# Optimization experiments

Measured on AMD Instinct MI355X. Metric: run time of the kernel, lower is better.

Reference implementation:

```python
import jax, jax.numpy as jnp
import numpy as np

N, CS, CZ = 512, 384, 128
H, C, PQ, PV = 12, 16, 4, 8
NB = 8
EPS = 1e-8


def _ln(x, g, b):
    m = jnp.mean(x, axis=-1, keepdims=True)
    v = jnp.mean((x - m) ** 2, axis=-1, keepdims=True)
    return (x - m) / jnp.sqrt(v + 1e-5) * g + b


def _quat_rot(bcd):
    # (1, b, c, d) quaternion -> rotation matrix, as in AF2 BackboneUpdate
    ones = jnp.ones(bcd.shape[:-1] + (1,), bcd.dtype)
    q = jnp.concatenate([ones, bcd], axis=-1)
    q = q / jnp.linalg.norm(q, axis=-1, keepdims=True)
    w, x, y, z = q[..., 0], q[..., 1], q[..., 2], q[..., 3]
    R = jnp.stack([
        1 - 2 * (y * y + z * z), 2 * (x * y - w * z), 2 * (x * z + w * y),
        2 * (x * y + w * z), 1 - 2 * (x * x + z * z), 2 * (y * z - w * x),
        2 * (x * z - w * y), 2 * (y * z + w * x), 1 - 2 * (x * x + y * y),
    ], axis=-1)
    return R.reshape(bcd.shape[:-1] + (3, 3))


def _ipa(s, z, R, t, p):
    n = s.shape[0]
    q = (s @ p['w_q']).reshape(n, H, C)
    kv = (s @ p['w_kv']).reshape(n, H, 2, C)
    k, v = kv[..., 0, :], kv[..., 1, :]

    # local points -> global frames
    q_pts = (s @ p['w_qpts']).reshape(n, H * PQ, 3)
    q_pts = jnp.einsum('nxy,npy->npx', R, q_pts) + t[:, None, :]
    q_pts = q_pts.reshape(n, H, PQ, 3)
    kv_pts = (s @ p['w_kvpts']).reshape(n, H * (PQ + PV), 3)
    kv_pts = jnp.einsum('nxy,npy->npx', R, kv_pts) + t[:, None, :]
    kv_pts = kv_pts.reshape(n, H, PQ + PV, 3)
    k_pts, v_pts = kv_pts[:, :, :PQ], kv_pts[:, :, PQ:]

    b = z @ p['w_b']  # [i, j, H]

    scalar = jnp.einsum('ihc,jhc->hij', q, k) / np.sqrt(C)
    # sum_p ||q_ip - k_jp||^2 expanded to avoid [N,N,H,P,3] intermediate
    sq_q = jnp.sum(q_pts ** 2, axis=(-1, -2)).T  # [H, i]
    sq_k = jnp.sum(k_pts ** 2, axis=(-1, -2)).T  # [H, j]
    cross = jnp.einsum('ihpc,jhpc->hij', q_pts, k_pts)
    d2 = sq_q[:, :, None] + sq_k[:, None, :] - 2.0 * cross  # [H, i, j]

    gamma = jax.nn.softplus(p['head_weights'])  # [H]
    w_C = np.sqrt(2.0 / (9.0 * PQ))
    w_L = np.sqrt(1.0 / 3.0)
    logits = w_L * (scalar + jnp.transpose(b, (2, 0, 1))
                    - gamma[:, None, None] * (w_C / 2.0) * d2)
    a = jax.nn.softmax(logits, axis=-1)  # [H, i, j]

    o = jnp.einsum('hij,jhc->ihc', a, v).reshape(n, H * C)
    o_pt = jnp.einsum('hij,jhpc->ihpc', a, v_pts)
    # back to local frame: R_i^{-1} (o_pt - t_i)
    o_pt = jnp.einsum('nyx,nhpy->nhpx', R, o_pt - t[:, None, None, :])
    o_pt_norm = jnp.sqrt(jnp.sum(o_pt ** 2, axis=-1) + EPS)  # [n, H, PV]
    o_pair = jnp.einsum('hij,ijz->ihz', a, z).reshape(n, H * CZ)

    cat = jnp.concatenate([o, o_pt.reshape(n, H * PV * 3),
                           o_pt_norm.reshape(n, H * PV), o_pair], axis=-1)
    return cat @ p['w_out'] + p['b_out']


def _forward(s, z, p):
    n = s.shape[0]
    R = jnp.broadcast_to(jnp.eye(3, dtype=s.dtype), (n, 3, 3))
    t = jnp.zeros((n, 3), s.dtype)
    for _ in range(NB):  # shared weights across blocks, as in AF2
        s = s + _ipa(s, z, R, t, p)
        s = _ln(s, p['ln1_g'], p['ln1_b'])
        h = jax.nn.relu(s @ p['w_t1'])
        h = jax.nn.relu(h @ p['w_t2'])
        s = s + h @ p['w_t3']
        s = _ln(s, p['ln2_g'], p['ln2_b'])
        upd = s @ p['w_bb'] + p['b_bb']  # [n, 6]
        Ru = _quat_rot(upd[:, :3])
        tu = upd[:, 3:]
        t = jnp.einsum('nxy,ny->nx', R, tu) + t
        R = jnp.einsum('nxy,nyz->nxz', R, Ru)
    return jnp.concatenate([s, t], axis=-1)  # [n, CS + 3]


def setup_inputs() -> dict:
    key = jax.random.key(0)
    ks = jax.random.split(key, 12)
    sc = 0.02
    cat_dim = H * C + H * PV * 3 + H * PV + H * CZ  # 2112
    return {
        's': jax.random.normal(ks[0], (N, CS), jnp.float32),
        'z': jax.random.normal(ks[1], (N, N, CZ), jnp.float32),
        'w_q': jax.random.normal(ks[2], (CS, H * C), jnp.float32) * sc,
        'w_kv': jax.random.normal(ks[3], (CS, H * 2 * C), jnp.float32) * sc,
        'w_qpts': jax.random.normal(ks[4], (CS, H * PQ * 3), jnp.float32) * sc,
        'w_kvpts': jax.random.normal(ks[5], (CS, H * (PQ + PV) * 3), jnp.float32) * sc,
        'w_b': jax.random.normal(ks[6], (CZ, H), jnp.float32) * sc,
        'head_weights': jnp.zeros((H,), jnp.float32),
        'w_out': jax.random.normal(ks[7], (cat_dim, CS), jnp.float32) * sc,
        'b_out': jnp.zeros((CS,), jnp.float32),
        'ln1_g': jnp.ones((CS,), jnp.float32),
        'ln1_b': jnp.zeros((CS,), jnp.float32),
        'w_t1': jax.random.normal(ks[8], (CS, CS), jnp.float32) * sc,
        'w_t2': jax.random.normal(ks[9], (CS, CS), jnp.float32) * sc,
        'w_t3': jax.random.normal(ks[10], (CS, CS), jnp.float32) * sc,
        'ln2_g': jnp.ones((CS,), jnp.float32),
        'ln2_b': jnp.zeros((CS,), jnp.float32),
        'w_bb': jax.random.normal(ks[11], (CS, 6), jnp.float32) * sc,
        'b_bb': jnp.zeros((6,), jnp.float32),
    }


def reference(s, z, w_q, w_kv, w_qpts, w_kvpts, w_b, head_weights, w_out,
              b_out, ln1_g, ln1_b, w_t1, w_t2, w_t3, ln2_g, ln2_b, w_bb, b_bb):
    p = dict(w_q=w_q, w_kv=w_kv, w_qpts=w_qpts, w_kvpts=w_kvpts, w_b=w_b,
             head_weights=head_weights, w_out=w_out, b_out=b_out,
             ln1_g=ln1_g, ln1_b=ln1_b, w_t1=w_t1, w_t2=w_t2, w_t3=w_t3,
             ln2_g=ln2_g, ln2_b=ln2_b, w_bb=w_bb, b_bb=b_bb)
    return _forward(s, z, p)
```

## Files before the change

kernel.cpp:

```cpp
#include <hip/hip_runtime.h>
#include <hip/hip_bf16.h>

constexpr int Nres = 512;
constexpr int Cs   = 384;
constexpr int Cz   = 128;
constexpr int NH   = 12;
constexpr int HC   = 16;
constexpr int NPQ  = 4;
constexpr int NPV  = 8;
constexpr int NBLK = 8;
constexpr int PROJD = NH*HC + NH*2*HC + NH*NPQ*3 + NH*(NPQ+NPV)*3;
constexpr int CATD = NH*HC + NH*NPV*3 + NH*NPV + NH*Cz;
constexpr float W_L  = 0.57735026918962576f;
constexpr float W_C2 = 0.11785113019775793f;

using u16 = unsigned short;
typedef __bf16 bf16x8 __attribute__((ext_vector_type(8)));
typedef float  f32x4  __attribute__((ext_vector_type(4)));

static inline int gdiv(int n, int b) { return (n + b - 1) / b; }

static __device__ __forceinline__ u16 f2bf(float x) {
    __hip_bfloat16 h = __float2bfloat16(x);
    return *reinterpret_cast<u16*>(&h);
}
static __device__ __forceinline__ float bf2f(u16 x) {
    return __bfloat162float(*reinterpret_cast<__hip_bfloat16*>(&x));
}

__global__ void k_init(const float* __restrict__ s_in, float* __restrict__ s_cur,
                       u16* __restrict__ s_bf,
                       float* __restrict__ R, float* __restrict__ t) {
    int idx = blockIdx.x * blockDim.x + threadIdx.x;
    if (idx < Nres * Cs) { float v = s_in[idx]; s_cur[idx] = v; s_bf[idx] = f2bf(v); }
    if (idx < Nres * 9) {
        int e = idx % 9;
        R[idx] = (e == 0 || e == 4 || e == 8) ? 1.f : 0.f;
    }
    if (idx < Nres * 3) t[idx] = 0.f;
}

__global__ void k_concatW(const float* __restrict__ w_q, const float* __restrict__ w_kv,
                          const float* __restrict__ w_qpts, const float* __restrict__ w_kvpts,
                          float* __restrict__ Wcat) {
    int idx = blockIdx.x * blockDim.x + threadIdx.x;
    if (idx >= Cs * PROJD) return;
    int k = idx / PROJD, n = idx - k * PROJD;
    float v;
    if      (n < 192) v = w_q[k * 192 + n];
    else if (n < 576) v = w_kv[k * 384 + (n - 192)];
    else if (n < 720) v = w_qpts[k * 144 + (n - 576)];
    else              v = w_kvpts[k * 432 + (n - 720)];
    Wcat[idx] = v;
}

__global__ void k_transposeW(const float* __restrict__ in, u16* __restrict__ out,
                             int K, int N) {
    __shared__ float tile[32][33];
    int n0 = blockIdx.x * 32, k0 = blockIdx.y * 32;
    int tx = threadIdx.x & 31, ty = threadIdx.x >> 5;
#pragma unroll
    for (int j = 0; j < 4; j++)
        tile[ty + j * 8][tx] = in[(size_t)(k0 + ty + j * 8) * N + n0 + tx];
    __syncthreads();
#pragma unroll
    for (int j = 0; j < 4; j++)
        out[(size_t)(n0 + ty + j * 8) * K + k0 + tx] = f2bf(tile[tx][ty + j * 8]);
}

__global__ void k_zT(const float* __restrict__ z, u16* __restrict__ zT) {
    __shared__ float tile[32][33];
    int i  = blockIdx.x;
    int j0 = blockIdx.y * 32;
    int c0 = blockIdx.z * 32;
    int tx = threadIdx.x & 31, ty = threadIdx.x >> 5;
    const float* src = z + (size_t)i * Nres * Cz;
#pragma unroll
    for (int l = 0; l < 4; l++)
        tile[ty + l * 8][tx] = src[(size_t)(j0 + ty + l * 8) * Cz + c0 + tx];
    __syncthreads();
    u16* dst = zT + (size_t)i * Cz * Nres;
#pragma unroll
    for (int l = 0; l < 4; l++)
        dst[(size_t)(c0 + ty + l * 8) * Nres + j0 + tx] = f2bf(tile[tx][ty + l * 8]);
}

__global__ void __launch_bounds__(256)
k_gemm_mfma(const u16* __restrict__ A, const u16* __restrict__ Bt,
            float* __restrict__ P, int M, int K, int N, int Kc) {
    __shared__ u16 As[2][64 * 40];
    __shared__ u16 Bs[2][64 * 40];
    const int tid = threadIdx.x;
    const int m0 = blockIdx.y * 64;
    const int n0 = blockIdx.x * 64;
    const int kbeg = blockIdx.z * Kc;
    const int kend = kbeg + Kc;
    const int wv = tid >> 6, lane = tid & 63;
    const int wm = (wv >> 1) * 32, wn = (wv & 1) * 32;
    const int lrow = lane & 15, lq = lane >> 4;

    f32x4 zero = {0.f, 0.f, 0.f, 0.f};
    f32x4 acc00 = zero, acc01 = zero, acc10 = zero, acc11 = zero;

    const int srow = tid >> 2;
    const int sko  = (tid & 3) * 8;
    const size_t aoff = (size_t)(m0 + srow) * K + sko;
    const size_t boff = (size_t)(n0 + srow) * K + sko;

    uint4 ra = *(const uint4*)&A[aoff + kbeg];
    uint4 rb = *(const uint4*)&Bt[boff + kbeg];
    *(uint4*)&As[0][srow * 40 + sko] = ra;
    *(uint4*)&Bs[0][srow * 40 + sko] = rb;
    __syncthreads();

    int buf = 0;
    for (int k0 = kbeg; k0 < kend; k0 += 32) {
        const bool nxt = (k0 + 32 < kend);
        if (nxt) {
            ra = *(const uint4*)&A[aoff + k0 + 32];
            rb = *(const uint4*)&Bt[boff + k0 + 32];
        }
        bf16x8 a0 = *reinterpret_cast<const bf16x8*>(&As[buf][(wm + lrow) * 40 + lq * 8]);
        bf16x8 a1 = *reinterpret_cast<const bf16x8*>(&As[buf][(wm + 16 + lrow) * 40 + lq * 8]);
        bf16x8 b0 = *reinterpret_cast<const bf16x8*>(&Bs[buf][(wn + lrow) * 40 + lq * 8]);
        bf16x8 b1 = *reinterpret_cast<const bf16x8*>(&Bs[buf][(wn + 16 + lrow) * 40 + lq * 8]);
        acc00 = __builtin_amdgcn_mfma_f32_16x16x32_bf16(a0, b0, acc00, 0, 0, 0);
        acc01 = __builtin_amdgcn_mfma_f32_16x16x32_bf16(a0, b1, acc01, 0, 0, 0);
        acc10 = __builtin_amdgcn_mfma_f32_16x16x32_bf16(a1, b0, acc10, 0, 0, 0);
        acc11 = __builtin_amdgcn_mfma_f32_16x16x32_bf16(a1, b1, acc11, 0, 0, 0);
        if (nxt) {
            *(uint4*)&As[buf ^ 1][srow * 40 + sko] = ra;
            *(uint4*)&Bs[buf ^ 1][srow * 40 + sko] = rb;
            __syncthreads();
            buf ^= 1;
        }
    }
    float* Pp = P + (size_t)blockIdx.z * M * N;
    const int rbase = m0 + wm + lq * 4;
    const int cbase = n0 + wn + lrow;
#pragma unroll
    for (int r = 0; r < 4; r++) {
        Pp[(size_t)(rbase + r) * N + cbase]           = acc00[r];
        Pp[(size_t)(rbase + r) * N + cbase + 16]      = acc01[r];
        Pp[(size_t)(rbase + 16 + r) * N + cbase]      = acc10[r];
        Pp[(size_t)(rbase + 16 + r) * N + cbase + 16] = acc11[r];
    }
}

__global__ void __launch_bounds__(256)
k_gemm_proj(const u16* __restrict__ A, const u16* __restrict__ Bt,
            float* __restrict__ outT, int M, int K, int N) {
    __shared__ u16 As[2][32 * 40];
    __shared__ u16 Bs[2][64 * 40];
    const int tid = threadIdx.x;
    const int m0 = blockIdx.y * 32;
    const int n0 = blockIdx.x * 64;
    const int wv = tid >> 6, lane = tid & 63;
    const int wm = (wv >> 1) * 16, wn = (wv & 1) * 32;
    const int lrow = lane & 15, lq = lane >> 4;
    f32x4 zero = {0.f, 0.f, 0.f, 0.f};
    f32x4 acc0 = zero, acc1 = zero;
    const int srow = tid >> 2, sko = (tid & 3) * 8;
    const size_t aoff = (size_t)(m0 + srow) * K + sko;
    const size_t boff = (size_t)(n0 + srow) * K + sko;

    uint4 ra, rb;
    if (tid < 128) ra = *(const uint4*)&A[aoff];
    rb = *(const uint4*)&Bt[boff];
    if (tid < 128) *(uint4*)&As[0][srow * 40 + sko] = ra;
    *(uint4*)&Bs[0][srow * 40 + sko] = rb;
    __syncthreads();

    int buf = 0;
    for (int k0 = 0; k0 < K; k0 += 32) {
        const bool nxt = (k0 + 32 < K);
        if (nxt) {
            if (tid < 128) ra = *(const uint4*)&A[aoff + k0 + 32];
            rb = *(const uint4*)&Bt[boff + k0 + 32];
        }
        bf16x8 a  = *reinterpret_cast<const bf16x8*>(&As[buf][(wm + lrow) * 40 + lq * 8]);
        bf16x8 b0 = *reinterpret_cast<const bf16x8*>(&Bs[buf][(wn + lrow) * 40 + lq * 8]);
        bf16x8 b1 = *reinterpret_cast<const bf16x8*>(&Bs[buf][(wn + 16 + lrow) * 40 + lq * 8]);
        acc0 = __builtin_amdgcn_mfma_f32_16x16x32_bf16(a, b0, acc0, 0, 0, 0);
        acc1 = __builtin_amdgcn_mfma_f32_16x16x32_bf16(a, b1, acc1, 0, 0, 0);
        if (nxt) {
            if (tid < 128) *(uint4*)&As[buf ^ 1][srow * 40 + sko] = ra;
            *(uint4*)&Bs[buf ^ 1][srow * 40 + sko] = rb;
            __syncthreads();
            buf ^= 1;
        }
    }
    const int rbase = m0 + wm + lq * 4;
    const int cbase = n0 + wn + lrow;
    *reinterpret_cast<f32x4*>(&outT[(size_t)cbase * M + rbase])        = acc0;
    *reinterpret_cast<f32x4*>(&outT[(size_t)(cbase + 16) * M + rbase]) = acc1;
}

__global__ void __launch_bounds__(256)
k_gemm_tr(const u16* __restrict__ Abf, const float* __restrict__ As0,
          const float* __restrict__ As1, const u16* __restrict__ Bt,
          float* __restrict__ Pout, int amode) {
    __shared__ u16 Asm[2][32 * 40];
    __shared__ u16 Bsm[2][64 * 40];
    const int tid = threadIdx.x;
    const int m0 = blockIdx.y * 32;
    const int n0 = blockIdx.x * 64;
    const int kbeg = blockIdx.z * 192;
    const int kend = kbeg + 192;
    const int wv = tid >> 6, lane = tid & 63;
    const int wm = (wv >> 1) * 16, wn = (wv & 1) * 32;
    const int lrow = lane & 15, lq = lane >> 4;
    f32x4 zero = {0.f, 0.f, 0.f, 0.f};
    f32x4 acc0 = zero, acc1 = zero;
    const int srow = tid >> 2, sko = (tid & 3) * 8;
    const int rowR = tid >> 3, c4 = (tid & 7) * 4;
    const size_t aoffb = (size_t)(m0 + srow) * Cs + sko;
    const size_t aoffr = (size_t)(m0 + rowR) * Cs + c4;
    const size_t boff  = (size_t)(n0 + srow) * Cs + sko;

    uint4 ra, rb;
    float4 f0, f1;
    rb = *(const uint4*)&Bt[boff + kbeg];
    if (amode == 0) { if (tid < 128) ra = *(const uint4*)&Abf[aoffb + kbeg]; }
    else { f0 = *(const float4*)&As0[aoffr + kbeg]; f1 = *(const float4*)&As1[aoffr + kbeg]; }

    if (amode == 0) { if (tid < 128) *(uint4*)&Asm[0][srow * 40 + sko] = ra; }
    else {
        uint2 wp;
        wp.x = (unsigned)f2bf(fmaxf(f0.x + f1.x, 0.f)) | ((unsigned)f2bf(fmaxf(f0.y + f1.y, 0.f)) << 16);
        wp.y = (unsigned)f2bf(fmaxf(f0.z + f1.z, 0.f)) | ((unsigned)f2bf(fmaxf(f0.w + f1.w, 0.f)) << 16);
        *(uint2*)&Asm[0][rowR * 40 + c4] = wp;
    }
    *(uint4*)&Bsm[0][srow * 40 + sko] = rb;
    __syncthreads();

    int buf = 0;
    for (int k0 = kbeg; k0 < kend; k0 += 32) {
        const bool nxt = (k0 + 32 < kend);
        if (nxt) {
            rb = *(const uint4*)&Bt[boff + k0 + 32];
            if (amode == 0) { if (tid < 128) ra = *(const uint4*)&Abf[aoffb + k0 + 32]; }
            else { f0 = *(const float4*)&As0[aoffr + k0 + 32]; f1 = *(const float4*)&As1[aoffr + k0 + 32]; }
        }
        bf16x8 a  = *reinterpret_cast<const bf16x8*>(&Asm[buf][(wm + lrow) * 40 + lq * 8]);
        bf16x8 b0 = *reinterpret_cast<const bf16x8*>(&Bsm[buf][(wn + lrow) * 40 + lq * 8]);
        bf16x8 b1 = *reinterpret_cast<const bf16x8*>(&Bsm[buf][(wn + 16 + lrow) * 40 + lq * 8]);
        acc0 = __builtin_amdgcn_mfma_f32_16x16x32_bf16(a, b0, acc0, 0, 0, 0);
        acc1 = __builtin_amdgcn_mfma_f32_16x16x32_bf16(a, b1, acc1, 0, 0, 0);
        if (nxt) {
            if (amode == 0) { if (tid < 128) *(uint4*)&Asm[buf ^ 1][srow * 40 + sko] = ra; }
            else {
                uint2 wp;
                wp.x = (unsigned)f2bf(fmaxf(f0.x + f1.x, 0.f)) | ((unsigned)f2bf(fmaxf(f0.y + f1.y, 0.f)) << 16);
                wp.y = (unsigned)f2bf(fmaxf(f0.z + f1.z, 0.f)) | ((unsigned)f2bf(fmaxf(f0.w + f1.w, 0.f)) << 16);
                *(uint2*)&Asm[buf ^ 1][rowR * 40 + c4] = wp;
            }
            *(uint4*)&Bsm[buf ^ 1][srow * 40 + sko] = rb;
            __syncthreads();
            buf ^= 1;
        }
    }
    float* Pp = Pout + (size_t)blockIdx.z * Nres * Cs;
    const int rbase = m0 + wm + lq * 4;
    const int cbase = n0 + wn + lrow;
#pragma unroll
    for (int r = 0; r < 4; r++) {
        Pp[(size_t)(rbase + r) * Cs + cbase]      = acc0[r];
        Pp[(size_t)(rbase + r) * Cs + cbase + 16] = acc1[r];
    }
}

__global__ void k_bproj(const float* __restrict__ z, const float* __restrict__ w_b,
                        u16* __restrict__ b_hij_bf) {
    __shared__ float zs[16][129];
    __shared__ float wbs[Cz * NH];
    const int tid = threadIdx.x;
    const int base = blockIdx.x * 16;
#pragma unroll
    for (int l = 0; l < 6; l++) {
        int idx = tid + l * 256;
        if (idx < Cz * NH) wbs[idx] = w_b[idx];
    }
#pragma unroll
    for (int l = 0; l < 8; l++) {
        int idx = tid + l * 256;
        int r = idx >> 7, c = idx & 127;
        zs[r][c] = z[(size_t)(base + r) * Cz + c];
    }
    __syncthreads();
    if (tid < 192) {
        int h = tid >> 4, r = tid & 15;
        float acc = 0.f;
        for (int c = 0; c < Cz; c++) acc += zs[r][c] * wbs[c * NH + h];
        int row = base + r;
        int i = row >> 9, j = row & 511;
        b_hij_bf[((size_t)h * Nres + i) * Nres + j] = f2bf(acc * W_L);
    }
}

__global__ void k_prep(const float* __restrict__ projT, const float* __restrict__ R,
                       const float* __restrict__ t, const float* __restrict__ hw,
                       u16* __restrict__ Aaug, u16* __restrict__ Baug,
                       u16* __restrict__ vhT) {
    int idx = blockIdx.x * blockDim.x + threadIdx.x;
    if (idx >= NH * Nres) return;
    int h = idx / Nres, i = idx % Nres;
#define PR(col) projT[(size_t)(col) * Nres + i]
    float R_[9], t_[3];
#pragma unroll
    for (int e = 0; e < 9; e++) R_[e] = R[i * 9 + e];
#pragma unroll
    for (int e = 0; e < 3; e++) t_[e] = t[i * 3 + e];
    float gam = log1pf(__expf(hw[h]));
    float ch  = sqrtf(2.f * gam * W_C2);

    u16 arow[32], brow[32];
#pragma unroll
    for (int c = 0; c < HC; c++) {
        arow[c] = f2bf(PR(h * HC + c) * (W_L * 0.25f));
        brow[c] = f2bf(PR(192 + h * 2 * HC + c));
        vhT[((size_t)h * 48 + c) * Nres + i] = f2bf(PR(192 + h * 2 * HC + HC + c));
    }
#pragma unroll
    for (int p = 0; p < NPQ; p++) {
        int c0 = 576 + (h * NPQ + p) * 3;
        float y0 = PR(c0 + 0), y1 = PR(c0 + 1), y2 = PR(c0 + 2);
        float v0 = R_[0]*y0 + R_[1]*y1 + R_[2]*y2 + t_[0];
        float v1 = R_[3]*y0 + R_[4]*y1 + R_[5]*y2 + t_[1];
        float v2 = R_[6]*y0 + R_[7]*y1 + R_[8]*y2 + t_[2];
        float s = W_L * ch;
        arow[16 + p*3 + 0] = f2bf(v0 * s);
        arow[16 + p*3 + 1] = f2bf(v1 * s);
        arow[16 + p*3 + 2] = f2bf(v2 * s);
    }
    float sk = 0.f;
#pragma unroll
    for (int p = 0; p < NPQ + NPV; p++) {
        int c0 = 720 + (h * (NPQ+NPV) + p) * 3;
        float y0 = PR(c0 + 0), y1 = PR(c0 + 1), y2 = PR(c0 + 2);
        float v0 = R_[0]*y0 + R_[1]*y1 + R_[2]*y2 + t_[0];
        float v1 = R_[3]*y0 + R_[4]*y1 + R_[5]*y2 + t_[1];
        float v2 = R_[6]*y0 + R_[7]*y1 + R_[8]*y2 + t_[2];
        if (p < NPQ) {
            brow[16 + p*3 + 0] = f2bf(v0 * ch);
            brow[16 + p*3 + 1] = f2bf(v1 * ch);
            brow[16 + p*3 + 2] = f2bf(v2 * ch);
            sk += v0*v0 + v1*v1 + v2*v2;
        } else {
            int cc = 16 + (p - NPQ) * 3;
            vhT[((size_t)h * 48 + cc + 0) * Nres + i] = f2bf(v0);
            vhT[((size_t)h * 48 + cc + 1) * Nres + i] = f2bf(v1);
            vhT[((size_t)h * 48 + cc + 2) * Nres + i] = f2bf(v2);
        }
    }
#undef PR
    float x = -W_L * gam * W_C2 * sk;
    u16 hi = f2bf(x);
    float lo = x - bf2f(hi);
    arow[28] = f2bf(1.0f); arow[29] = f2bf(1.0f); arow[30] = 0; arow[31] = 0;
    brow[28] = hi;         brow[29] = f2bf(lo);   brow[30] = 0; brow[31] = 0;

    uint4* ad = (uint4*)&Aaug[((size_t)h * Nres + i) * 32];
    uint4* bd = (uint4*)&Baug[((size_t)h * Nres + i) * 32];
    const uint4* as = (const uint4*)arow;
    const uint4* bs = (const uint4*)brow;
#pragma unroll
    for (int e = 0; e < 4; e++) { ad[e] = as[e]; bd[e] = bs[e]; }
}

__global__ void __launch_bounds__(256)
k_attn(const u16* __restrict__ Aaug, const u16* __restrict__ Baug,
       const u16* __restrict__ b_hij_bf, const u16* __restrict__ vhT,
       const float* __restrict__ R, const float* __restrict__ t,
       u16* __restrict__ Pbf, u16* __restrict__ cat_bf) {
    __shared__ union {
        struct { u16 A[64 * 40]; u16 B[512 * 40]; } qk;
        u16 P[64 * 520];
    } U;
    __shared__ u16 Bsv[2][48 * 40];
    __shared__ float Ct[64 * 49];

    const int i0 = blockIdx.x * 64;
    const int h  = blockIdx.y;
    const int tid = threadIdx.x;
    const int wv = tid >> 6, lane = tid & 63;
    const int lrow = lane & 15, lq = lane >> 4;
    const int wm = wv * 16;
    const int srow = tid >> 2, sko = (tid & 3) * 8;

    const u16* Bp = vhT + (size_t)h * 48 * Nres;
    const size_t boff = (size_t)srow * Nres + sko;
    if (tid < 192) {
        uint4 rv = *(const uint4*)&Bp[boff];
        *(uint4*)&Bsv[0][srow * 40 + sko] = rv;
    }

    {
        int r4 = tid >> 2, q = tid & 3;
        *(uint4*)&U.qk.A[r4 * 40 + q * 8] =
            *(const uint4*)&Aaug[((size_t)h * Nres + i0 + r4) * 32 + q * 8];
#pragma unroll
        for (int l = 0; l < 8; l++) {
            int idx = tid + l * 256;
            int rr = idx >> 2, qq = idx & 3;
            *(uint4*)&U.qk.B[rr * 40 + qq * 8] =
                *(const uint4*)&Baug[((size_t)h * Nres + rr) * 32 + qq * 8];
        }
    }
    __syncthreads();

    f32x4 zero = {0.f, 0.f, 0.f, 0.f};
    bf16x8 afrag = *reinterpret_cast<const bf16x8*>(&U.qk.A[(wm + lrow) * 40 + lq * 8]);
    f32x4 acc[32];
#pragma unroll
    for (int tt = 0; tt < 32; tt++) {
        bf16x8 bfr = *reinterpret_cast<const bf16x8*>(&U.qk.B[(tt * 16 + lrow) * 40 + lq * 8]);
        acc[tt] = __builtin_amdgcn_mfma_f32_16x16x32_bf16(afrag, bfr, zero, 0, 0, 0);
    }
    __syncthreads();

    {
        const u16* bhp = b_hij_bf + ((size_t)h * Nres + i0) * Nres;
#pragma unroll
        for (int l = 0; l < 16; l++) {
            int v = tid + l * 256;
            int rr = v >> 6, cq = v & 63;
            *(uint4*)&U.P[rr * 520 + cq * 8] =
                *(const uint4*)&bhp[(size_t)rr * Nres + cq * 8];
        }
    }
    __syncthreads();

#pragma unroll
    for (int tt = 0; tt < 32; tt++) {
#pragma unroll
        for (int r = 0; r < 4; r++)
            acc[tt][r] += bf2f(U.P[(wm + lq * 4 + r) * 520 + tt * 16 + lrow]);
    }

    float mx[4] = {-1e30f, -1e30f, -1e30f, -1e30f};
#pragma unroll
    for (int tt = 0; tt < 32; tt++)
#pragma unroll
        for (int r = 0; r < 4; r++) mx[r] = fmaxf(mx[r], acc[tt][r]);
#pragma unroll
    for (int off = 8; off > 0; off >>= 1)
#pragma unroll
        for (int r = 0; r < 4; r++) mx[r] = fmaxf(mx[r], __shfl_xor(mx[r], off));
    float sm[4] = {0.f, 0.f, 0.f, 0.f};
#pragma unroll
    for (int tt = 0; tt < 32; tt++)
#pragma unroll
        for (int r = 0; r < 4; r++) { acc[tt][r] = __expf(acc[tt][r] - mx[r]); sm[r] += acc[tt][r]; }
#pragma unroll
    for (int off = 8; off > 0; off >>= 1)
#pragma unroll
        for (int r = 0; r < 4; r++) sm[r] += __shfl_xor(sm[r], off);
    float inv[4];
#pragma unroll
    for (int r = 0; r < 4; r++) inv[r] = 1.f / sm[r];

    __syncthreads();

#pragma unroll
    for (int tt = 0; tt < 32; tt++)
#pragma unroll
        for (int r = 0; r < 4; r++)
            U.P[(wm + lq * 4 + r) * 520 + tt * 16 + lrow] = f2bf(acc[tt][r] * inv[r]);
    __syncthreads();

#pragma unroll
    for (int l = 0; l < 16; l++) {
        int v = tid + l * 256;
        int rr = v >> 6, cq = v & 63;
        *(uint4*)&Pbf[((size_t)h * Nres + i0 + rr) * 512 + cq * 8] =
            *(const uint4*)&U.P[rr * 520 + cq * 8];
    }

    f32x4 o0 = zero, o1 = zero, o2 = zero;
    int buf = 0;
    for (int k0 = 0; k0 < Nres; k0 += 32) {
        const bool nxt = (k0 + 32 < Nres);
        uint4 rv;
        if (nxt && tid < 192) rv = *(const uint4*)&Bp[boff + k0 + 32];
        bf16x8 a  = *reinterpret_cast<const bf16x8*>(&U.P[(wm + lrow) * 520 + k0 + lq * 8]);
        bf16x8 b0 = *reinterpret_cast<const bf16x8*>(&Bsv[buf][(lrow) * 40 + lq * 8]);
        bf16x8 b1 = *reinterpret_cast<const bf16x8*>(&Bsv[buf][(16 + lrow) * 40 + lq * 8]);
        bf16x8 b2 = *reinterpret_cast<const bf16x8*>(&Bsv[buf][(32 + lrow) * 40 + lq * 8]);
        o0 = __builtin_amdgcn_mfma_f32_16x16x32_bf16(a, b0, o0, 0, 0, 0);
        o1 = __builtin_amdgcn_mfma_f32_16x16x32_bf16(a, b1, o1, 0, 0, 0);
        o2 = __builtin_amdgcn_mfma_f32_16x16x32_bf16(a, b2, o2, 0, 0, 0);
        if (nxt) {
            if (tid < 192) *(uint4*)&Bsv[buf ^ 1][srow * 40 + sko] = rv;
            __syncthreads();
            buf ^= 1;
        }
    }
#pragma unroll
    for (int r = 0; r < 4; r++) {
        int row = wm + lq * 4 + r;
        Ct[row * 49 + lrow]      = o0[r];
        Ct[row * 49 + 16 + lrow] = o1[r];
        Ct[row * 49 + 32 + lrow] = o2[r];
    }
    __syncthreads();
#pragma unroll
    for (int l = 0; l < 4; l++) {
        int idx = tid + l * 256;
        int r = idx >> 4, c = idx & 15;
        cat_bf[(size_t)(i0 + r) * CATD + h * HC + c] = f2bf(Ct[r * 49 + c]);
    }
#pragma unroll
    for (int l = 0; l < 2; l++) {
        int idx = tid + l * 256;
        int r = idx >> 3, p = idx & 7;
        int i = i0 + r;
        float g0 = Ct[r * 49 + 16 + p * 3 + 0];
        float g1 = Ct[r * 49 + 16 + p * 3 + 1];
        float g2 = Ct[r * 49 + 16 + p * 3 + 2];
        float d0 = g0 - t[i * 3 + 0], d1 = g1 - t[i * 3 + 1], d2v = g2 - t[i * 3 + 2];
        const float* Rn = R + i * 9;
        float l0 = Rn[0] * d0 + Rn[3] * d1 + Rn[6] * d2v;
        float l1 = Rn[1] * d0 + Rn[4] * d1 + Rn[7] * d2v;
        float l2 = Rn[2] * d0 + Rn[5] * d1 + Rn[8] * d2v;
        int hp = h * NPV + p;
        u16* crow = cat_bf + (size_t)i * CATD;
        crow[192 + hp * 3 + 0] = f2bf(l0);
        crow[192 + hp * 3 + 1] = f2bf(l1);
        crow[192 + hp * 3 + 2] = f2bf(l2);
        crow[480 + hp] = f2bf(sqrtf(l0 * l0 + l1 * l1 + l2 * l2 + 1e-8f));
    }
}

__global__ void __launch_bounds__(256)
k_opair(const u16* __restrict__ Pbf, const u16* __restrict__ zT,
        u16* __restrict__ cat_bf) {
    __shared__ u16 P_lds[16 * 520];
    __shared__ u16 Bs[2][128 * 40];
    const int i = blockIdx.x;
    const int tid = threadIdx.x;
    const int wv = tid >> 6, ln = tid & 63;
    const int srow = tid >> 2, sko = (tid & 3) * 8;
    const u16* Bp = zT + (size_t)i * Cz * Nres;
    const size_t b0off = (size_t)srow * Nres + sko;
    const size_t b1off = (size_t)(64 + srow) * Nres + sko;

    uint4 rb0 = *(const uint4*)&Bp[b0off];
    uint4 rb1 = *(const uint4*)&Bp[b1off];

#pragma unroll
    for (int l = 0; l < 3; l++) {
        int v = tid + l * 256;
        int hh = v >> 6, cq = v & 63;
        *(uint4*)&P_lds[hh * 520 + cq * 8] =
            *(const uint4*)&Pbf[((size_t)hh * Nres + i) * 512 + cq * 8];
    }
    for (int l = tid; l < 4 * 520; l += 256) P_lds[12 * 520 + l] = 0;

    *(uint4*)&Bs[0][srow * 40 + sko]        = rb0;
    *(uint4*)&Bs[0][(64 + srow) * 40 + sko] = rb1;
    __syncthreads();

    const int lrow = ln & 15, lq = ln >> 4;
    const int wn = wv * 32;
    f32x4 zero = {0.f, 0.f, 0.f, 0.f};
    f32x4 acc0 = zero, acc1 = zero;
    int buf = 0;
    for (int k0 = 0; k0 < Nres; k0 += 32) {
        const bool nxt = (k0 + 32 < Nres);
        if (nxt) {
            rb0 = *(const uint4*)&Bp[b0off + k0 + 32];
            rb1 = *(const uint4*)&Bp[b1off + k0 + 32];
        }
        bf16x8 a  = *reinterpret_cast<const bf16x8*>(&P_lds[lrow * 520 + k0 + lq * 8]);
        bf16x8 b0 = *reinterpret_cast<const bf16x8*>(&Bs[buf][(wn + lrow) * 40 + lq * 8]);
        bf16x8 b1 = *reinterpret_cast<const bf16x8*>(&Bs[buf][(wn + 16 + lrow) * 40 + lq * 8]);
        acc0 = __builtin_amdgcn_mfma_f32_16x16x32_bf16(a, b0, acc0, 0, 0, 0);
        acc1 = __builtin_amdgcn_mfma_f32_16x16x32_bf16(a, b1, acc1, 0, 0, 0);
        if (nxt) {
            *(uint4*)&Bs[buf ^ 1][srow * 40 + sko]        = rb0;
            *(uint4*)&Bs[buf ^ 1][(64 + srow) * 40 + sko] = rb1;
            __syncthreads();
            buf ^= 1;
        }
    }
    u16* crow = cat_bf + (size_t)i * CATD + 576;
#pragma unroll
    for (int r = 0; r < 4; r++) {
        int row = lq * 4 + r;
        if (row < NH) {
            crow[row * Cz + wn + lrow]      = f2bf(acc0[r]);
            crow[row * Cz + wn + 16 + lrow] = f2bf(acc1[r]);
        }
    }
}

__global__ void k_reduce_ln(const float* __restrict__ P, const float* __restrict__ bias,
                            float* __restrict__ s, u16* __restrict__ s_bf,
                            const float* __restrict__ g, const float* __restrict__ b,
                            int nsplit) {
    __shared__ float red[512];
    int i = blockIdx.x, tid = threadIdx.x;
    float v = s[(size_t)i * Cs + tid];
    if (bias) v += bias[tid];
    for (int sp = 0; sp < nsplit; sp++) v += P[(size_t)sp * Nres * Cs + (size_t)i * Cs + tid];
    red[tid] = v;
    if (tid < 128) red[384 + tid] = 0.f;
    __syncthreads();
    for (int st = 256; st > 0; st >>= 1) { if (tid < st) red[tid] += red[tid + st]; __syncthreads(); }
    float mean = red[0] / Cs;
    __syncthreads();
    float d = v - mean;
    red[tid] = d * d;
    if (tid < 128) red[384 + tid] = 0.f;
    __syncthreads();
    for (int st = 256; st > 0; st >>= 1) { if (tid < st) red[tid] += red[tid + st]; __syncthreads(); }
    float var = red[0] / Cs;
    float o = d * rsqrtf(var + 1e-5f) * g[tid] + b[tid];
    s[(size_t)i * Cs + tid] = o;
    s_bf[(size_t)i * Cs + tid] = f2bf(o);
}

__global__ void k_reduce_ln_bb(const float* __restrict__ P, float* __restrict__ s,
                               u16* __restrict__ s_bf,
                               const float* __restrict__ g, const float* __restrict__ b,
                               int nsplit,
                               const float* __restrict__ w_bb, const float* __restrict__ b_bb,
                               float* __restrict__ R, float* __restrict__ t) {
    __shared__ float red[512];
    __shared__ float uw[36];
    int i = blockIdx.x, tid = threadIdx.x;
    float v = s[(size_t)i * Cs + tid];
    for (int sp = 0; sp < nsplit; sp++) v += P[(size_t)sp * Nres * Cs + (size_t)i * Cs + tid];
    red[tid] = v;
    if (tid < 128) red[384 + tid] = 0.f;
    __syncthreads();
    for (int st = 256; st > 0; st >>= 1) { if (tid < st) red[tid] += red[tid + st]; __syncthreads(); }
    float mean = red[0] / Cs;
    __syncthreads();
    float d = v - mean;
    red[tid] = d * d;
    if (tid < 128) red[384 + tid] = 0.f;
    __syncthreads();
    for (int st = 256; st > 0; st >>= 1) { if (tid < st) red[tid] += red[tid + st]; __syncthreads(); }
    float var = red[0] / Cs;
    float o = d * rsqrtf(var + 1e-5f) * g[tid] + b[tid];
    s[(size_t)i * Cs + tid] = o;
    s_bf[(size_t)i * Cs + tid] = f2bf(o);

    float u[6];
#pragma unroll
    for (int dd = 0; dd < 6; dd++) u[dd] = o * w_bb[tid * 6 + dd];
#pragma unroll
    for (int off = 32; off > 0; off >>= 1)
#pragma unroll
        for (int dd = 0; dd < 6; dd++) u[dd] += __shfl_xor(u[dd], off);
    int wv = tid >> 6, lane = tid & 63;
    if (lane == 0) {
#pragma unroll
        for (int dd = 0; dd < 6; dd++) uw[wv * 6 + dd] = u[dd];
    }
    __syncthreads();
    if (tid == 0) {
        float uu[6];
#pragma unroll
        for (int dd = 0; dd < 6; dd++) {
            float a = b_bb[dd];
            for (int w = 0; w < 6; w++) a += uw[w * 6 + dd];
            uu[dd] = a;
        }
        float qb = uu[0], qc = uu[1], qd = uu[2];
        float inv = rsqrtf(1.f + qb*qb + qc*qc + qd*qd);
        float w = inv, x = qb * inv, y = qc * inv, zq = qd * inv;
        float Ru[9] = {
            1.f - 2.f*(y*y + zq*zq), 2.f*(x*y - w*zq),       2.f*(x*zq + w*y),
            2.f*(x*y + w*zq),        1.f - 2.f*(x*x + zq*zq), 2.f*(y*zq - w*x),
            2.f*(x*zq - w*y),        2.f*(y*zq + w*x),        1.f - 2.f*(x*x + y*y)
        };
        float Ro[9];
#pragma unroll
        for (int e = 0; e < 9; e++) Ro[e] = R[i * 9 + e];
        float tu0 = uu[3], tu1 = uu[4], tu2 = uu[5];
        t[i*3+0] += Ro[0]*tu0 + Ro[1]*tu1 + Ro[2]*tu2;
        t[i*3+1] += Ro[3]*tu0 + Ro[4]*tu1 + Ro[5]*tu2;
        t[i*3+2] += Ro[6]*tu0 + Ro[7]*tu1 + Ro[8]*tu2;
#pragma unroll
        for (int r = 0; r < 3; r++)
#pragma unroll
            for (int c = 0; c < 3; c++)
                R[i*9 + r*3 + c] = Ro[r*3+0]*Ru[0*3+c] + Ro[r*3+1]*Ru[1*3+c] + Ro[r*3+2]*Ru[2*3+c];
    }
}

__global__ void k_final(const float* __restrict__ s, const float* __restrict__ t,
                        float* __restrict__ out) {
    int idx = blockIdx.x * blockDim.x + threadIdx.x;
    if (idx >= Nres * (Cs + 3)) return;
    int i = idx / (Cs + 3), c = idx - i * (Cs + 3);
    out[idx] = (c < Cs) ? s[(size_t)i * Cs + c] : t[i * 3 + (c - Cs)];
}

extern "C" void kernel_launch(void* const* d_in, const int* in_sizes, int n_in,
                              void* d_out, int out_size, void* d_ws, size_t ws_size,
                              hipStream_t stream) {
    const float* s_in    = (const float*)d_in[0];
    const float* z       = (const float*)d_in[1];
    const float* w_q     = (const float*)d_in[2];
    const float* w_kv    = (const float*)d_in[3];
    const float* w_qpts  = (const float*)d_in[4];
    const float* w_kvpts = (const float*)d_in[5];
    const float* w_b     = (const float*)d_in[6];
    const float* hw      = (const float*)d_in[7];
    const float* w_out   = (const float*)d_in[8];
    const float* b_out   = (const float*)d_in[9];
    const float* ln1_g   = (const float*)d_in[10];
    const float* ln1_b   = (const float*)d_in[11];
    const float* w_t1    = (const float*)d_in[12];
    const float* w_t2    = (const float*)d_in[13];
    const float* w_t3    = (const float*)d_in[14];
    const float* ln2_g   = (const float*)d_in[15];
    const float* ln2_b   = (const float*)d_in[16];
    const float* w_bb    = (const float*)d_in[17];
    const float* b_bb    = (const float*)d_in[18];
    float* out = (float*)d_out;

    float* ws = (float*)d_ws;
    size_t off = 0;
    float* s_cur = ws + off; off += (size_t)Nres * Cs;
    float* projT = ws + off; off += (size_t)Nres * PROJD;
    float* Wcat  = ws + off; off += (size_t)Cs * PROJD;
    float* Rbuf  = ws + off; off += (size_t)Nres * 9;
    float* tbuf  = ws + off; off += (size_t)Nres * 3;
    float* Pslab = ws + off; off += (size_t)11 * Nres * Cs;
    u16* b_hij_bf = (u16*)(ws + off); off += (size_t)NH * Nres * Nres / 2;
    u16* s_bf   = (u16*)(ws + off); off += (size_t)Nres * Cs / 2;
    u16* cat_bf = (u16*)(ws + off); off += (size_t)Nres * CATD / 2;
    u16* WcatT  = (u16*)(ws + off); off += (size_t)Cs * PROJD / 2;
    u16* w_outT = (u16*)(ws + off); off += (size_t)CATD * Cs / 2;
    u16* w_t1T  = (u16*)(ws + off); off += (size_t)Cs * Cs / 2;
    u16* w_t2T  = (u16*)(ws + off); off += (size_t)Cs * Cs / 2;
    u16* w_t3T  = (u16*)(ws + off); off += (size_t)Cs * Cs / 2;
    u16* Pbf    = (u16*)(ws + off); off += (size_t)NH * Nres * Nres / 2;
    u16* vhTbf  = (u16*)(ws + off); off += (size_t)NH * 48 * Nres / 2;
    u16* Aaug   = (u16*)(ws + off); off += (size_t)NH * Nres * 32 / 2;
    u16* Baug   = (u16*)(ws + off); off += (size_t)NH * Nres * 32 / 2;
    u16* zTbf   = (u16*)(ws + off); off += (size_t)Nres * Cz * Nres / 2;

    const int MNs = Nres * Cs;

    k_init<<<gdiv(Nres*Cs, 256), 256, 0, stream>>>(s_in, s_cur, s_bf, Rbuf, tbuf);
    k_concatW<<<gdiv(Cs*PROJD, 256), 256, 0, stream>>>(w_q, w_kv, w_qpts, w_kvpts, Wcat);
    k_transposeW<<<dim3(PROJD/32, Cs/32), 256, 0, stream>>>(Wcat, WcatT, Cs, PROJD);
    k_transposeW<<<dim3(Cs/32, CATD/32), 256, 0, stream>>>(w_out, w_outT, CATD, Cs);
    k_transposeW<<<dim3(Cs/32, Cs/32), 256, 0, stream>>>(w_t1, w_t1T, Cs, Cs);
    k_transposeW<<<dim3(Cs/32, Cs/32), 256, 0, stream>>>(w_t2, w_t2T, Cs, Cs);
    k_transposeW<<<dim3(Cs/32, Cs/32), 256, 0, stream>>>(w_t3, w_t3T, Cs, Cs);
    k_bproj<<<Nres*Nres/16, 256, 0, stream>>>(z, w_b, b_hij_bf);
    k_zT<<<dim3(Nres, Nres/32, Cz/32), 256, 0, stream>>>(z, zTbf);

    for (int it = 0; it < NBLK; it++) {
        k_gemm_proj<<<dim3(PROJD/64, Nres/32), 256, 0, stream>>>(s_bf, WcatT, projT, Nres, Cs, PROJD);
        k_prep<<<gdiv(NH*Nres, 256), 256, 0, stream>>>(projT, Rbuf, tbuf, hw, Aaug, Baug, vhTbf);
        k_attn<<<dim3(Nres/64, NH), 256, 0, stream>>>(Aaug, Baug, b_hij_bf, vhTbf, Rbuf, tbuf, Pbf, cat_bf);
        k_opair<<<Nres, 256, 0, stream>>>(Pbf, zTbf, cat_bf);
        k_gemm_mfma<<<dim3(Cs/64, Nres/64, 6), 256, 0, stream>>>(cat_bf, w_outT, Pslab, Nres, CATD, Cs, 352);
        k_reduce_ln<<<Nres, Cs, 0, stream>>>(Pslab, b_out, s_cur, s_bf, ln1_g, ln1_b, 6);
        k_gemm_tr<<<dim3(Cs/64, Nres/32, 2), 256, 0, stream>>>(s_bf, nullptr, nullptr, w_t1T, Pslab, 0);
        k_gemm_tr<<<dim3(Cs/64, Nres/32, 2), 256, 0, stream>>>(nullptr, Pslab, Pslab + MNs, w_t2T, Pslab + 2*MNs, 1);
        k_gemm_tr<<<dim3(Cs/64, Nres/32, 2), 256, 0, stream>>>(nullptr, Pslab + 2*MNs, Pslab + 3*MNs, w_t3T, Pslab + 4*MNs, 1);
        k_reduce_ln_bb<<<Nres, Cs, 0, stream>>>(Pslab + 4*MNs, s_cur, s_bf, ln2_g, ln2_b, 2, w_bb, b_bb, Rbuf, tbuf);
    }

    k_final<<<gdiv(Nres*(Cs+3), 256), 256, 0, stream>>>(s_cur, tbuf, out);
}
```

Baseline: 896.1 us.

## Shrink attention row tile to 16 and split keys across waves; fuse final output write

The attention kernel now handles 16 query rows per block instead of 64. Each of its four waves covers a 128-key slice, with cross-wave softmax max/sum reductions and partial PV accumulators combined through shared memory. This gives four times as many blocks, improving occupancy and cutting LDS use, and K/V fragments are read straight from global memory instead of being staged. Separately, the last layer-norm/backbone kernel writes the final output directly, which removes the k_final launch. The costs are extra barriers and redundant global reads of K and V per block.

```diff
diff --git a/kernel.cpp b/kernel.cpp
--- a/kernel.cpp
+++ b/kernel.cpp
@@ -373,151 +373,143 @@
        const u16* __restrict__ b_hij_bf, const u16* __restrict__ vhT,
        const float* __restrict__ R, const float* __restrict__ t,
        u16* __restrict__ Pbf, u16* __restrict__ cat_bf) {
-    __shared__ union {
-        struct { u16 A[64 * 40]; u16 B[512 * 40]; } qk;
-        u16 P[64 * 520];
-    } U;
-    __shared__ u16 Bsv[2][48 * 40];
-    __shared__ float Ct[64 * 49];
-
-    const int i0 = blockIdx.x * 64;
+    __shared__ u16 P_lds[16 * 520];
+    __shared__ float Ctp[4][16 * 49];
+    __shared__ float sred[4][32];
+
+    const int i0 = blockIdx.x * 16;
     const int h  = blockIdx.y;
     const int tid = threadIdx.x;
-    const int wv = tid >> 6, lane = tid & 63;
+    const int w = tid >> 6, lane = tid & 63;
     const int lrow = lane & 15, lq = lane >> 4;
-    const int wm = wv * 16;
-    const int srow = tid >> 2, sko = (tid & 3) * 8;
-
-    const u16* Bp = vhT + (size_t)h * 48 * Nres;
-    const size_t boff = (size_t)srow * Nres + sko;
-    if (tid < 192) {
-        uint4 rv = *(const uint4*)&Bp[boff];
-        *(uint4*)&Bsv[0][srow * 40 + sko] = rv;
-    }
-
-    {
-        int r4 = tid >> 2, q = tid & 3;
-        *(uint4*)&U.qk.A[r4 * 40 + q * 8] =
-            *(const uint4*)&Aaug[((size_t)h * Nres + i0 + r4) * 32 + q * 8];
-#pragma unroll
-        for (int l = 0; l < 8; l++) {
-            int idx = tid + l * 256;
-            int rr = idx >> 2, qq = idx & 3;
-            *(uint4*)&U.qk.B[rr * 40 + qq * 8] =
-                *(const uint4*)&Baug[((size_t)h * Nres + rr) * 32 + qq * 8];
-        }
-    }
-    __syncthreads();
-
+    const int jbase = w * 128;
+
+    const u16* bhp = b_hij_bf + ((size_t)h * Nres + i0) * Nres;
+    uint4 bhreg[4];
+#pragma unroll
+    for (int l = 0; l < 4; l++) {
+        int v = tid + l * 256;
+        int rr = v >> 6, cq = v & 63;
+        bhreg[l] = *(const uint4*)&bhp[(size_t)rr * Nres + cq * 8];
+    }
+
+    bf16x8 afrag = *reinterpret_cast<const bf16x8*>(
+        &Aaug[((size_t)h * Nres + i0 + lrow) * 32 + lq * 8]);
     f32x4 zero = {0.f, 0.f, 0.f, 0.f};
-    bf16x8 afrag = *reinterpret_cast<const bf16x8*>(&U.qk.A[(wm + lrow) * 40 + lq * 8]);
-    f32x4 acc[32];
-#pragma unroll
-    for (int tt = 0; tt < 32; tt++) {
-        bf16x8 bfr = *reinterpret_cast<const bf16x8*>(&U.qk.B[(tt * 16 + lrow) * 40 + lq * 8]);
+    f32x4 acc[8];
+#pragma unroll
+    for (int tt = 0; tt < 8; tt++) {
+        bf16x8 bfr = *reinterpret_cast<const bf16x8*>(
+            &Baug[((size_t)h * Nres + jbase + tt * 16 + lrow) * 32 + lq * 8]);
         acc[tt] = __builtin_amdgcn_mfma_f32_16x16x32_bf16(afrag, bfr, zero, 0, 0, 0);
     }
-    __syncthreads();
-
-    {
-        const u16* bhp = b_hij_bf + ((size_t)h * Nres + i0) * Nres;
-#pragma unroll
-        for (int l = 0; l < 16; l++) {
-            int v = tid + l * 256;
-            int rr = v >> 6, cq = v & 63;
-            *(uint4*)&U.P[rr * 520 + cq * 8] =
-                *(const uint4*)&bhp[(size_t)rr * Nres + cq * 8];
-        }
-    }
-    __syncthreads();
-
-#pragma unroll
-    for (int tt = 0; tt < 32; tt++) {
+
+#pragma unroll
+    for (int l = 0; l < 4; l++) {
+        int v = tid + l * 256;
+        int rr = v >> 6, cq = v & 63;
+        *(uint4*)&P_lds[rr * 520 + cq * 8] = bhreg[l];
+    }
+    __syncthreads();
+#pragma unroll
+    for (int tt = 0; tt < 8; tt++)
 #pragma unroll
         for (int r = 0; r < 4; r++)
-            acc[tt][r] += bf2f(U.P[(wm + lq * 4 + r) * 520 + tt * 16 + lrow]);
-    }
-
-    float mx[4] = {-1e30f, -1e30f, -1e30f, -1e30f};
-#pragma unroll
-    for (int tt = 0; tt < 32; tt++)
-#pragma unroll
-        for (int r = 0; r < 4; r++) mx[r] = fmaxf(mx[r], acc[tt][r]);
+            acc[tt][r] += bf2f(P_lds[(lq * 4 + r) * 520 + jbase + tt * 16 + lrow]);
+
+    float pmx[4] = {-1e30f, -1e30f, -1e30f, -1e30f};
+#pragma unroll
+    for (int tt = 0; tt < 8; tt++)
+#pragma unroll
+        for (int r = 0; r < 4; r++) pmx[r] = fmaxf(pmx[r], acc[tt][r]);
 #pragma unroll
     for (int off = 8; off > 0; off >>= 1)
 #pragma unroll
-        for (int r = 0; r < 4; r++) mx[r] = fmaxf(mx[r], __shfl_xor(mx[r], off));
-    float sm[4] = {0.f, 0.f, 0.f, 0.f};
-#pragma unroll
-    for (int tt = 0; tt < 32; tt++)
-#pragma unroll
-        for (int r = 0; r < 4; r++) { acc[tt][r] = __expf(acc[tt][r] - mx[r]); sm[r] += acc[tt][r]; }
+        for (int r = 0; r < 4; r++) pmx[r] = fmaxf(pmx[r], __shfl_xor(pmx[r], off));
+    if (lrow == 0) {
+#pragma unroll
+        for (int r = 0; r < 4; r++) sred[w][lq * 4 + r] = pmx[r];
+    }
+    __syncthreads();
+    float mx[4];
+#pragma unroll
+    for (int r = 0; r < 4; r++) {
+        int row = lq * 4 + r;
+        mx[r] = fmaxf(fmaxf(sred[0][row], sred[1][row]), fmaxf(sred[2][row], sred[3][row]));
+    }
+    float psm[4] = {0.f, 0.f, 0.f, 0.f};
+#pragma unroll
+    for (int tt = 0; tt < 8; tt++)
+#pragma unroll
+        for (int r = 0; r < 4; r++) { acc[tt][r] = __expf(acc[tt][r] - mx[r]); psm[r] += acc[tt][r]; }
 #pragma unroll
     for (int off = 8; off > 0; off >>= 1)
 #pragma unroll
-        for (int r = 0; r < 4; r++) sm[r] += __shfl_xor(sm[r], off);
+        for (int r = 0; r < 4; r++) psm[r] += __shfl_xor(psm[r], off);
+    if (lrow == 0) {
+#pragma unroll
+        for (int r = 0; r < 4; r++) sred[w][16 + lq * 4 + r] = psm[r];
+    }
+    __syncthreads();
     float inv[4];
 #pragma unroll
-    for (int r = 0; r < 4; r++) inv[r] = 1.f / sm[r];
-
-    __syncthreads();
-
-#pragma unroll
-    for (int tt = 0; tt < 32; tt++)
+    for (int r = 0; r < 4; r++) {
+        int row = 16 + lq * 4 + r;
+        inv[r] = 1.f / (sred[0][row] + sred[1][row] + sred[2][row] + sred[3][row]);
+    }
+
+#pragma unroll
+    for (int tt = 0; tt < 8; tt++)
 #pragma unroll
         for (int r = 0; r < 4; r++)
-            U.P[(wm + lq * 4 + r) * 520 + tt * 16 + lrow] = f2bf(acc[tt][r] * inv[r]);
-    __syncthreads();
-
-#pragma unroll
-    for (int l = 0; l < 16; l++) {
+            P_lds[(lq * 4 + r) * 520 + jbase + tt * 16 + lrow] = f2bf(acc[tt][r] * inv[r]);
+    __syncthreads();
+
+#pragma unroll
+    for (int l = 0; l < 4; l++) {
         int v = tid + l * 256;
         int rr = v >> 6, cq = v & 63;
         *(uint4*)&Pbf[((size_t)h * Nres + i0 + rr) * 512 + cq * 8] =
-            *(const uint4*)&U.P[rr * 520 + cq * 8];
-    }
-
+            *(const uint4*)&P_lds[rr * 520 + cq * 8];
+    }
+
+    const u16* Bvp = vhT + (size_t)h * 48 * Nres;
     f32x4 o0 = zero, o1 = zero, o2 = zero;
-    int buf = 0;
-    for (int k0 = 0; k0 < Nres; k0 += 32) {
-        const bool nxt = (k0 + 32 < Nres);
-        uint4 rv;
-        if (nxt && tid < 192) rv = *(const uint4*)&Bp[boff + k0 + 32];
-        bf16x8 a  = *reinterpret_cast<const bf16x8*>(&U.P[(wm + lrow) * 520 + k0 + lq * 8]);
-        bf16x8 b0 = *reinterpret_cast<const bf16x8*>(&Bsv[buf][(lrow) * 40 + lq * 8]);
-        bf16x8 b1 = *reinterpret_cast<const bf16x8*>(&Bsv[buf][(16 + lrow) * 40 + lq * 8]);
-        bf16x8 b2 = *reinterpret_cast<const bf16x8*>(&Bsv[buf][(32 + lrow) * 40 + lq * 8]);
+#pragma unroll
+    for (int s = 0; s < 4; s++) {
+        int k0 = w * 128 + s * 32;
+        bf16x8 a  = *reinterpret_cast<const bf16x8*>(&P_lds[lrow * 520 + k0 + lq * 8]);
+        bf16x8 b0 = *reinterpret_cast<const bf16x8*>(&Bvp[(size_t)(lrow) * Nres + k0 + lq * 8]);
+        bf16x8 b1 = *reinterpret_cast<const bf16x8*>(&Bvp[(size_t)(16 + lrow) * Nres + k0 + lq * 8]);
+        bf16x8 b2 = *reinterpret_cast<const bf16x8*>(&Bvp[(size_t)(32 + lrow) * Nres + k0 + lq * 8]);
         o0 = __builtin_amdgcn_mfma_f32_16x16x32_bf16(a, b0, o0, 0, 0, 0);
         o1 = __builtin_amdgcn_mfma_f32_16x16x32_bf16(a, b1, o1, 0, 0, 0);
         o2 = __builtin_amdgcn_mfma_f32_16x16x32_bf16(a, b2, o2, 0, 0, 0);
-        if (nxt) {
-            if (tid < 192) *(uint4*)&Bsv[buf ^ 1][srow * 40 + sko] = rv;
-            __syncthreads();
-            buf ^= 1;
-        }
     }
 #pragma unroll
     for (int r = 0; r < 4; r++) {
-        int row = wm + lq * 4 + r;
-        Ct[row * 49 + lrow]      = o0[r];
-        Ct[row * 49 + 16 + lrow] = o1[r];
-        Ct[row * 49 + 32 + lrow] = o2[r];
-    }
-    __syncthreads();
-#pragma unroll
-    for (int l = 0; l < 4; l++) {
-        int idx = tid + l * 256;
-        int r = idx >> 4, c = idx & 15;
-        cat_bf[(size_t)(i0 + r) * CATD + h * HC + c] = f2bf(Ct[r * 49 + c]);
-    }
-#pragma unroll
-    for (int l = 0; l < 2; l++) {
-        int idx = tid + l * 256;
-        int r = idx >> 3, p = idx & 7;
+        int row = lq * 4 + r;
+        Ctp[w][row * 49 + lrow]      = o0[r];
+        Ctp[w][row * 49 + 16 + lrow] = o1[r];
+        Ctp[w][row * 49 + 32 + lrow] = o2[r];
+    }
+    __syncthreads();
+
+    {
+        int r = tid >> 4, c = tid & 15;
+        float v = Ctp[0][r * 49 + c] + Ctp[1][r * 49 + c] + Ctp[2][r * 49 + c] + Ctp[3][r * 49 + c];
+        cat_bf[(size_t)(i0 + r) * CATD + h * HC + c] = f2bf(v);
+    }
+    if (tid < 128) {
+        int r = tid >> 3, p = tid & 7;
         int i = i0 + r;
-        float g0 = Ct[r * 49 + 16 + p * 3 + 0];
-        float g1 = Ct[r * 49 + 16 + p * 3 + 1];
-        float g2 = Ct[r * 49 + 16 + p * 3 + 2];
+        float g0 = 0.f, g1 = 0.f, g2 = 0.f;
+#pragma unroll
+        for (int ww = 0; ww < 4; ww++) {
+            g0 += Ctp[ww][r * 49 + 16 + p * 3 + 0];
+            g1 += Ctp[ww][r * 49 + 16 + p * 3 + 1];
+            g2 += Ctp[ww][r * 49 + 16 + p * 3 + 2];
+        }
         float d0 = g0 - t[i * 3 + 0], d1 = g1 - t[i * 3 + 1], d2v = g2 - t[i * 3 + 2];
         const float* Rn = R + i * 9;
         float l0 = Rn[0] * d0 + Rn[3] * d1 + Rn[6] * d2v;
@@ -626,7 +618,8 @@
                                const float* __restrict__ g, const float* __restrict__ b,
                                int nsplit,
                                const float* __restrict__ w_bb, const float* __restrict__ b_bb,
-                               float* __restrict__ R, float* __restrict__ t) {
+                               float* __restrict__ R, float* __restrict__ t,
+                               float* __restrict__ outbuf) {
     __shared__ float red[512];
     __shared__ float uw[36];
     int i = blockIdx.x, tid = threadIdx.x;
@@ -647,6 +640,7 @@
     float o = d * rsqrtf(var + 1e-5f) * g[tid] + b[tid];
     s[(size_t)i * Cs + tid] = o;
     s_bf[(size_t)i * Cs + tid] = f2bf(o);
+    if (outbuf) outbuf[(size_t)i * (Cs + 3) + tid] = o;
 
     float u[6];
 #pragma unroll
@@ -681,23 +675,21 @@
 #pragma unroll
         for (int e = 0; e < 9; e++) Ro[e] = R[i * 9 + e];
         float tu0 = uu[3], tu1 = uu[4], tu2 = uu[5];
-        t[i*3+0] += Ro[0]*tu0 + Ro[1]*tu1 + Ro[2]*tu2;
-        t[i*3+1] += Ro[3]*tu0 + Ro[4]*tu1 + Ro[5]*tu2;
-        t[i*3+2] += Ro[6]*tu0 + Ro[7]*tu1 + Ro[8]*tu2;
+        float t0 = t[i*3+0] + Ro[0]*tu0 + Ro[1]*tu1 + Ro[2]*tu2;
+        float t1 = t[i*3+1] + Ro[3]*tu0 + Ro[4]*tu1 + Ro[5]*tu2;
+        float t2 = t[i*3+2] + Ro[6]*tu0 + Ro[7]*tu1 + Ro[8]*tu2;
+        t[i*3+0] = t0; t[i*3+1] = t1; t[i*3+2] = t2;
+        if (outbuf) {
+            outbuf[(size_t)i * (Cs + 3) + Cs + 0] = t0;
+            outbuf[(size_t)i * (Cs + 3) + Cs + 1] = t1;
+            outbuf[(size_t)i * (Cs + 3) + Cs + 2] = t2;
+        }
 #pragma unroll
         for (int r = 0; r < 3; r++)
 #pragma unroll
             for (int c = 0; c < 3; c++)
                 R[i*9 + r*3 + c] = Ro[r*3+0]*Ru[0*3+c] + Ro[r*3+1]*Ru[1*3+c] + Ro[r*3+2]*Ru[2*3+c];
     }
-}
-
-__global__ void k_final(const float* __restrict__ s, const float* __restrict__ t,
-                        float* __restrict__ out) {
-    int idx = blockIdx.x * blockDim.x + threadIdx.x;
-    if (idx >= Nres * (Cs + 3)) return;
-    int i = idx / (Cs + 3), c = idx - i * (Cs + 3);
-    out[idx] = (c < Cs) ? s[(size_t)i * Cs + c] : t[i * 3 + (c - Cs)];
 }
 
 extern "C" void kernel_launch(void* const* d_in, const int* in_sizes, int n_in,
@@ -761,15 +753,15 @@
     for (int it = 0; it < NBLK; it++) {
         k_gemm_proj<<<dim3(PROJD/64, Nres/32), 256, 0, stream>>>(s_bf, WcatT, projT, Nres, Cs, PROJD);
         k_prep<<<gdiv(NH*Nres, 256), 256, 0, stream>>>(projT, Rbuf, tbuf, hw, Aaug, Baug, vhTbf);
-        k_attn<<<dim3(Nres/64, NH), 256, 0, stream>>>(Aaug, Baug, b_hij_bf, vhTbf, Rbuf, tbuf, Pbf, cat_bf);
+        k_attn<<<dim3(Nres/16, NH), 256, 0, stream>>>(Aaug, Baug, b_hij_bf, vhTbf, Rbuf, tbuf, Pbf, cat_bf);
         k_opair<<<Nres, 256, 0, stream>>>(Pbf, zTbf, cat_bf);
         k_gemm_mfma<<<dim3(Cs/64, Nres/64, 6), 256, 0, stream>>>(cat_bf, w_outT, Pslab, Nres, CATD, Cs, 352);
         k_reduce_ln<<<Nres, Cs, 0, stream>>>(Pslab, b_out, s_cur, s_bf, ln1_g, ln1_b, 6);
         k_gemm_tr<<<dim3(Cs/64, Nres/32, 2), 256, 0, stream>>>(s_bf, nullptr, nullptr, w_t1T, Pslab, 0);
         k_gemm_tr<<<dim3(Cs/64, Nres/32, 2), 256, 0, stream>>>(nullptr, Pslab, Pslab + MNs, w_t2T, Pslab + 2*MNs, 1);
         k_gemm_tr<<<dim3(Cs/64, Nres/32, 2), 256, 0, stream>>>(nullptr, Pslab + 2*MNs, Pslab + 3*MNs, w_t3T, Pslab + 4*MNs, 1);
-        k_reduce_ln_bb<<<Nres, Cs, 0, stream>>>(Pslab + 4*MNs, s_cur, s_bf, ln2_g, ln2_b, 2, w_bb, b_bb, Rbuf, tbuf);
-    }
-
-    k_final<<<gdiv(Nres*(Cs+3), 256), 256, 0, stream>>>(s_cur, tbuf, out);
-}
+        k_reduce_ln_bb<<<Nres, Cs, 0, stream>>>(Pslab + 4*MNs, s_cur, s_bf, ln2_g, ln2_b, 2,
+                                                w_bb, b_bb, Rbuf, tbuf,
+                                                (it == NBLK - 1) ? out : nullptr);
+    }
+}
```

Result: faster. 852.1 us (-4.9%).
